# Performance work log

Measured on AMD Instinct MI355X. Metric: run time of the kernel, lower is better.

## Reference

```python
import jax, jax.numpy as jnp
import numpy as np
from jax import lax

# config (matches init_kwargs)
NUM_CLASSES = 10
SCORE_THRESH = 0.05
TOPK = 1000
DET_PER_IMG = 100
NMS_SCORE = 0.3
NMS_SIGMA = 0.5
IMG_H, IMG_W = 800.0, 1333.0
IOU_SUPPRESS = 0.8
BBOX_XFORM_CLIP = float(np.log(1000.0 / 16.0))
EPS = 1e-7


def setup_inputs() -> dict:
    key = jax.random.key(0)
    k1, k2, k3 = jax.random.split(key, 3)
    B, A, C = 8, 200000, NUM_CLASSES
    cls_logits = jax.random.normal(k1, (B, A, C), dtype=jnp.float32)
    bbox_regression = 0.5 * jax.random.normal(k2, (B, A, 4), dtype=jnp.float32)
    # plausible anchors: random centers + sizes inside the image, xyxy format
    u = jax.random.uniform(k3, (A, 6), dtype=jnp.float32)
    cx = u[:, 0] * IMG_W
    cy = u[:, 1] * IMG_H
    w = 16.0 + u[:, 2] * 200.0
    h = 16.0 + u[:, 3] * 200.0
    anchors = jnp.stack([cx - 0.5 * w, cy - 0.5 * h, cx + 0.5 * w, cy + 0.5 * h], axis=-1)
    return {"cls_logits": cls_logits, "bbox_regression": bbox_regression, "anchors": anchors}


def _decode(rel, anc):
    # torchvision BoxCoder.decode_single, weights (1,1,1,1). rel, anc: [K,4] xyxy anchors
    wa = anc[:, 2] - anc[:, 0]
    ha = anc[:, 3] - anc[:, 1]
    cxa = anc[:, 0] + 0.5 * wa
    cya = anc[:, 1] + 0.5 * ha
    dx, dy = rel[:, 0], rel[:, 1]
    dw = jnp.minimum(rel[:, 2], BBOX_XFORM_CLIP)
    dh = jnp.minimum(rel[:, 3], BBOX_XFORM_CLIP)
    cx = dx * wa + cxa
    cy = dy * ha + cya
    w = jnp.exp(dw) * wa
    h = jnp.exp(dh) * ha
    boxes = jnp.stack([cx - 0.5 * w, cy - 0.5 * h, cx + 0.5 * w, cy + 0.5 * h], axis=-1)
    # clip_boxes_to_image
    x = jnp.clip(boxes[:, 0::2], 0.0, IMG_W)
    y = jnp.clip(boxes[:, 1::2], 0.0, IMG_H)
    return jnp.stack([x[:, 0], y[:, 0], x[:, 1], y[:, 1]], axis=-1)


def _iou_one(box, boxes):
    # box [4] vs boxes [K,4] -> [K]
    lt = jnp.maximum(box[:2], boxes[:, :2])
    rb = jnp.minimum(box[2:], boxes[:, 2:])
    wh = jnp.clip(rb - lt, 0.0)
    inter = wh[:, 0] * wh[:, 1]
    a1 = (box[2] - box[0]) * (box[3] - box[1])
    a2 = (boxes[:, 2] - boxes[:, 0]) * (boxes[:, 3] - boxes[:, 1])
    return inter / (a1 + a2 - inter + EPS)


def _postprocess_one(logits, rel, anchors):
    # logits [A,C], rel [A,4], anchors [A,4]
    probs = jax.nn.sigmoid(logits)
    scores_all = jnp.max(probs, axis=-1)               # [A]
    labels_all = jnp.argmax(probs, axis=-1)            # [A]
    scores_all = jnp.where(scores_all > SCORE_THRESH, scores_all, 0.0)
    top_scores, top_idx = lax.top_k(scores_all, TOPK)  # [K]
    labels = labels_all[top_idx]
    boxes = _decode(rel[top_idx], anchors[top_idx])    # [K,4]

    K = TOPK
    # --- batched gaussian soft-NMS (same-label decay only) ---
    def soft_step(carry, _):
        sc, out = carry
        i = jnp.argmax(sc)
        s = sc[i]
        out = out.at[i].set(jnp.maximum(s, 0.0))
        ious = _iou_one(boxes[i], boxes)
        decay = jnp.where(labels == labels[i], jnp.exp(-(ious ** 2) / NMS_SIGMA), 1.0)
        sc = (sc * decay).at[i].set(-1.0)
        return (sc, out), None
    (_, decayed), _ = lax.scan(soft_step, (top_scores, jnp.zeros_like(top_scores)), None, length=K)
    keep = decayed > NMS_SCORE

    # --- sort by decayed score desc, greedy hard suppression at IoU>0.8 ---
    order = jnp.argsort(-decayed)
    b = boxes[order]
    s = decayed[order]
    l = labels[order]
    alive0 = keep[order]
    idxs = jnp.arange(K)

    def greedy_step(alive, i):
        ious = _iou_one(b[i], b)
        suppress = (ious > IOU_SUPPRESS) & (idxs > i)
        alive = jnp.where(alive[i], alive & ~suppress, alive)
        return alive, None
    alive, _ = lax.scan(greedy_step, alive0, idxs)

    final_scores = jnp.where(alive, s, -1.0)
    out_scores, out_i = lax.top_k(final_scores, DET_PER_IMG)  # preserves desc order of survivors
    return b[out_i], out_scores, l[out_i]


def reference(cls_logits, bbox_regression, anchors):
    boxes, scores, labels = jax.vmap(_postprocess_one, in_axes=(0, 0, None))(
        cls_logits, bbox_regression, anchors)
    return boxes, scores, labels  # [B,D,4], [B,D], [B,D] (score -1 = padding)
```

## Files before the change

### kernel.cpp

```cpp
#include <hip/hip_runtime.h>
#include <math.h>

#define NCLS 10
#define TOPK 1000
#define DETS 100
#define CANDMAX 4096
#define SLOTS 16
#define ACTK 256

#define NB2 256
#define MGATE (-2.9444389791664403f)
#define SEAM 2.2f
#define SCA 30.907200f
#define SCB 41.0f
#define NBLK 64

__device__ __forceinline__ float sigmoidf_(float x) {
    return 1.0f / (1.0f + expf(-x));
}

__device__ __forceinline__ int mbin_(float m) {
    if (!(m > MGATE)) return 0;
    int b;
    if (m > SEAM) { b = 161 + (int)((m - SEAM) * SCB); if (b > 255) b = 255; }
    else          { b = 1 + (int)((m - MGATE) * SCA);  if (b > 160) b = 160; }
    return b;
}

__device__ __forceinline__ float key_score(const unsigned long long* key, int c) {
    return __uint_as_float(~(unsigned)(key[c] >> 32));
}

__device__ __forceinline__ unsigned fkey_(float f) {
    unsigned b = __float_as_uint(f);
    return (b & 0x80000000u) ? ~b : (b | 0x80000000u);
}
__device__ __forceinline__ float funkey_(unsigned k) {
    return __uint_as_float((k & 0x80000000u) ? (k & 0x7FFFFFFFu) : ~k);
}

__device__ __forceinline__ unsigned wave_umax_(unsigned x) {
    unsigned t;
    t = (unsigned)__builtin_amdgcn_update_dpp(0, (int)x, 0x111, 0xF, 0xF, false); x = (x > t) ? x : t;
    t = (unsigned)__builtin_amdgcn_update_dpp(0, (int)x, 0x112, 0xF, 0xF, false); x = (x > t) ? x : t;
    t = (unsigned)__builtin_amdgcn_update_dpp(0, (int)x, 0x114, 0xF, 0xF, false); x = (x > t) ? x : t;
    t = (unsigned)__builtin_amdgcn_update_dpp(0, (int)x, 0x118, 0xF, 0xF, false); x = (x > t) ? x : t;
    t = (unsigned)__builtin_amdgcn_update_dpp(0, (int)x, 0x142, 0xF, 0xF, false); x = (x > t) ? x : t;
    t = (unsigned)__builtin_amdgcn_update_dpp(0, (int)x, 0x143, 0xF, 0xF, false); x = (x > t) ? x : t;
    return (unsigned)__builtin_amdgcn_readlane((int)x, 63);
}

__global__ __launch_bounds__(256) void k_score_bins(const float* __restrict__ logits,
                                                    unsigned char* __restrict__ binc,
                                                    unsigned* hist,
                                                    unsigned* __restrict__ done,
                                                    unsigned* __restrict__ P,
                                                    int A) {
    __shared__ unsigned h[4][NB2];
    __shared__ int s_last;
    int img = blockIdx.y;
    for (int i = threadIdx.x; i < 4 * NB2; i += 256) ((unsigned*)h)[i] = 0;
    __syncthreads();

    const float* base = logits + (size_t)img * A * NCLS;
    unsigned char* bc = binc + (size_t)img * A;
    int rep = threadIdx.x & 3;
    int nquad = A >> 2;
    for (int q = blockIdx.x * 256 + threadIdx.x; q < nquad; q += NBLK * 256) {
        const float4* lp = (const float4*)(base + (size_t)q * 40);
        float f[40];
#pragma unroll
        for (int i = 0; i < 10; ++i) ((float4*)f)[i] = lp[i];
        unsigned ub = 0;
#pragma unroll
        for (int j = 0; j < 4; ++j) {
            float m = f[10 * j];
#pragma unroll
            for (int c = 1; c < 10; ++c) m = fmaxf(m, f[10 * j + c]);
            int b = mbin_(m);
            ub |= ((unsigned)b) << (8 * j);
            if (b) atomicAdd(&h[rep][b], 1u);
        }
        *(unsigned*)(bc + (size_t)q * 4) = ub;
    }
    int tail0 = nquad << 2;
    if (blockIdx.x == 0) {
        for (int a = tail0 + (int)threadIdx.x; a < A; a += 256) {
            const float* lp2 = base + (size_t)a * NCLS;
            float m = lp2[0];
            for (int c = 1; c < 10; ++c) m = fmaxf(m, lp2[c]);
            int b = mbin_(m);
            bc[a] = (unsigned char)b;
            if (b) atomicAdd(&h[rep][b], 1u);
        }
    }
    __syncthreads();
    for (int i = threadIdx.x; i < NB2; i += 256) {
        unsigned c = h[0][i] + h[1][i] + h[2][i] + h[3][i];
        if (c) atomicAdd(&hist[(size_t)img * NB2 + i], c);
    }
    __syncthreads();
    if (threadIdx.x == 0) {
        __threadfence();
        unsigned old = atomicAdd(&done[img], 1u);
        s_last = (old == (unsigned)(NBLK - 1)) ? 1 : 0;
    }
    __syncthreads();
    if (s_last && threadIdx.x < 64) {
        int lane = threadIdx.x;
        unsigned* hh = hist + (size_t)img * NB2;
        unsigned b4[4];
        unsigned s = 0;
#pragma unroll
        for (int j = 0; j < 4; ++j) { b4[j] = atomicAdd(&hh[lane * 4 + j], 0u); s += b4[j]; }
        unsigned suf = s;
#pragma unroll
        for (int d = 1; d < 64; d <<= 1) {
            unsigned o = __shfl_down(suf, d);
            if (lane + d < 64) suf += o;
        }
        unsigned above = __shfl_down(suf, 1);
        if (lane == 63) above = 0;
        if (lane == 0 && suf < (unsigned)TOPK) P[img] = 0u;
        if (above < (unsigned)TOPK && suf >= (unsigned)TOPK) {
            unsigned cum = above;
            for (int j = 3; j >= 0; --j) {
                cum += b4[j];
                if (cum >= (unsigned)TOPK) { P[img] = (unsigned)(lane * 4 + j); break; }
            }
        }
    }
}

__global__ __launch_bounds__(256) void k_compact(const float* __restrict__ logits,
                                                 const unsigned char* __restrict__ binc,
                                                 const unsigned* __restrict__ P,
                                                 unsigned* __restrict__ ctr,
                                                 unsigned long long* __restrict__ cand,
                                                 int A) {
    int img = blockIdx.y;
    unsigned p = P[img];
    unsigned psel = p ? (p - 1u) : 0u;
    int lane = threadIdx.x & 63;
    const float* base = logits + (size_t)img * A * NCLS;
    const unsigned* b4 = (const unsigned*)(binc + (size_t)img * A);
    int nquad = A >> 2;
    for (int q = blockIdx.x * 256 + threadIdx.x; q < nquad; q += NBLK * 256) {
        unsigned ub = b4[q];
#pragma unroll
        for (int j = 0; j < 4; ++j) {
            unsigned bj = (ub >> (8 * j)) & 0xFFu;
            bool take = (psel == 0u) || (bj >= psel);
            unsigned long long mask = __ballot(take);
            if (mask) {
                int cnt = __popcll(mask);
                int leader = __ffsll((unsigned long long)mask) - 1;
                unsigned pos = 0;
                if (lane == leader) pos = atomicAdd(&ctr[img], (unsigned)cnt);
                pos = (unsigned)__shfl((int)pos, leader);
                if (take) {
                    unsigned slot = pos + (unsigned)__popcll(mask & ((1ull << lane) - 1ull));
                    if (slot < CANDMAX) {
                        unsigned a = (unsigned)(q * 4 + j);
                        const float* lp = base + (size_t)a * NCLS;
                        float m = lp[0];
#pragma unroll
                        for (int c = 1; c < 10; ++c) m = fmaxf(m, lp[c]);
                        float sc = sigmoidf_(m);
                        sc = (sc > 0.05f) ? sc : 0.0f;
                        unsigned bits = __float_as_uint(sc);
                        cand[(size_t)img * CANDMAX + slot] =
                            ((unsigned long long)bits << 32) | (unsigned)(~a);
                    }
                }
            }
        }
    }
    int tail0 = nquad << 2;
    if (blockIdx.x == 0) {
        for (int a = tail0 + (int)threadIdx.x; a < A; a += 256) {
            unsigned bj = binc[(size_t)img * A + a];
            if ((psel == 0u) || (bj >= psel)) {
                const float* lp = base + (size_t)a * NCLS;
                float m = lp[0];
                for (int c = 1; c < 10; ++c) m = fmaxf(m, lp[c]);
                float sc = sigmoidf_(m);
                sc = (sc > 0.05f) ? sc : 0.0f;
                unsigned bits = __float_as_uint(sc);
                unsigned pos = atomicAdd(&ctr[img], 1u);
                if (pos < CANDMAX)
                    cand[(size_t)img * CANDMAX + pos] =
                        ((unsigned long long)bits << 32) | (unsigned)(~a);
            }
        }
    }
}

__global__ __launch_bounds__(1024) void k_sortnms(const unsigned long long* __restrict__ cand,
                                                  const unsigned* __restrict__ ctr,
                                                  const float* __restrict__ logits,
                                                  const float* __restrict__ rel,
                                                  const float* __restrict__ anch,
                                                  float* __restrict__ out, int A, int B) {
    __shared__ unsigned long long key[CANDMAX];
    __shared__ float s_box[TOPK][4];
    __shared__ int   s_lab[TOPK];
    __shared__ float s_pbox[TOPK][4];
    __shared__ int   s_plab[TOPK];
    __shared__ float s_psc[TOPK];
    __shared__ int   s_alive[TOPK];

    const float CLIPV = 4.135166556742356f;
    const float EPS = 1e-7f;
    const float W_ = 1333.0f, H_ = 800.0f;

    int img = blockIdx.x;
    int tid = threadIdx.x;

    unsigned n = ctr[img];
    if (n > CANDMAX) n = CANDMAX;
    int L = (n <= 1024) ? 1024 : (n <= 2048) ? 2048 : CANDMAX;
    for (int i = tid; i < L; i += 1024)
        key[i] = (i < (int)n) ? ~cand[(size_t)img * CANDMAX + i] : ~0ull;
    __syncthreads();
    for (int k = 2; k <= L; k <<= 1) {
        for (int j = k >> 1; j > 0; j >>= 1) {
            for (int i = tid; i < L; i += 1024) {
                int l = i ^ j;
                if (l > i) {
                    unsigned long long va = key[i], vb = key[l];
                    bool up = ((i & k) == 0);
                    if (up ? (va > vb) : (va < vb)) { key[i] = vb; key[l] = va; }
                }
            }
            __syncthreads();
        }
    }
    for (int i = L + tid; i < CANDMAX; i += 1024) key[i] = ~0ull;
    __syncthreads();

    if (tid < TOPK) {
        unsigned long long ik = key[tid];
        unsigned ai = (unsigned)ik;
        if (ai >= (unsigned)A) ai = 0;
        const float* lp = logits + ((size_t)img * A + ai) * NCLS;
        float best = sigmoidf_(lp[0]); int lbb = 0;
#pragma unroll
        for (int cc = 1; cc < NCLS; ++cc) {
            float v = sigmoidf_(lp[cc]);
            if (v > best) { best = v; lbb = cc; }
        }
        const float* rp = rel + ((size_t)img * A + ai) * 4;
        const float* ap = anch + (size_t)ai * 4;
        float a0 = ap[0], a1 = ap[1], a2 = ap[2], a3 = ap[3];
        float wa = a2 - a0, ha = a3 - a1;
        float cxa = a0 + 0.5f * wa, cya = a1 + 0.5f * ha;
        float dx = rp[0], dy = rp[1];
        float dw = fminf(rp[2], CLIPV), dh = fminf(rp[3], CLIPV);
        float cx = dx * wa + cxa, cy = dy * ha + cya;
        float w = expf(dw) * wa, h = expf(dh) * ha;
        s_box[tid][0] = fminf(fmaxf(cx - 0.5f * w, 0.0f), W_);
        s_box[tid][1] = fminf(fmaxf(cy - 0.5f * h, 0.0f), H_);
        s_box[tid][2] = fminf(fmaxf(cx + 0.5f * w, 0.0f), W_);
        s_box[tid][3] = fminf(fmaxf(cy + 0.5f * h, 0.0f), H_);
        s_lab[tid] = lbb;
    }
    __syncthreads();
    if (tid >= 64) return;
    int lane = tid;

    int M = TOPK;
    int need_full = 0;
    float bound = key_score(key, ACTK);

    {
        float sc[4], x1[4], y1[4], x2[4], y2[4], ar[4];
        int lb[4];
#pragma unroll
        for (int j = 0; j < 4; ++j) {
            int c = lane + (j << 6);
            float4 bb = *(const float4*)&s_box[c][0];
            x1[j] = bb.x; y1[j] = bb.y; x2[j] = bb.z; y2[j] = bb.w;
            ar[j] = (bb.z - bb.x) * (bb.w - bb.y);
            lb[j] = s_lab[c];
            sc[j] = key_score(key, c);
        }

        int nconf = 0, Mf = -1;

        for (int t = 0; t < ACTK; ++t) {
            float bv = sc[0]; int bj = 0;
#pragma unroll
            for (int j = 1; j < 4; ++j)
                if (sc[j] > bv) { bv = sc[j]; bj = j; }
            unsigned mk = fkey_(bv);
            unsigned mx = wave_umax_(mk);
            float pcur = funkey_(mx);

            if (!(pcur >= bound)) { need_full = 1; break; }

            int pick = -1;
#pragma unroll
            for (int jj = 0; jj < 4; ++jj) {
                if (pick < 0) {
                    unsigned long long mj = __ballot(mk == mx && bj == jj);
                    if (mj) pick = (jj << 6) + (__ffsll(mj) - 1);
                }
            }

            int jw = pick >> 6, wl = pick & 63;
            float xs = x1[0], ys = y1[0], zs = x2[0], ws = y2[0]; int ls = lb[0];
            if (jw == 1) { xs = x1[1]; ys = y1[1]; zs = x2[1]; ws = y2[1]; ls = lb[1]; }
            if (jw == 2) { xs = x1[2]; ys = y1[2]; zs = x2[2]; ws = y2[2]; ls = lb[2]; }
            if (jw == 3) { xs = x1[3]; ys = y1[3]; zs = x2[3]; ws = y2[3]; ls = lb[3]; }
            float4 pb;
            pb.x = __int_as_float(__builtin_amdgcn_readlane(__float_as_int(xs), wl));
            pb.y = __int_as_float(__builtin_amdgcn_readlane(__float_as_int(ys), wl));
            pb.z = __int_as_float(__builtin_amdgcn_readlane(__float_as_int(zs), wl));
            pb.w = __int_as_float(__builtin_amdgcn_readlane(__float_as_int(ws), wl));
            int plab_ = __builtin_amdgcn_readlane(ls, wl);

            float psc = fmaxf(pcur, 0.0f);
            if (lane == 0) {
                *(float4*)&s_pbox[t][0] = pb;
                s_plab[t] = plab_;
                s_psc[t] = psc;
            }

            float4 qb[4]; int ga[4];
#pragma unroll
            for (int k = 0; k < 4; ++k) {
                int p = lane + (k << 6);
                int pc2 = (p < t) ? p : 0;
                qb[k] = *(const float4*)&s_pbox[pc2][0];
                ga[k] = (p < t) ? s_alive[pc2] : 0;
            }

            float wax = (pb.z - pb.x) * (pb.w - pb.y);
#pragma unroll
            for (int j = 0; j < 4; ++j) {
                float lx2 = fmaxf(pb.x, x1[j]), ly2 = fmaxf(pb.y, y1[j]);
                float rx2 = fminf(pb.z, x2[j]), ry2 = fminf(pb.w, y2[j]);
                float iw2 = fmaxf(rx2 - lx2, 0.0f), ih2 = fmaxf(ry2 - ly2, 0.0f);
                float inter2 = iw2 * ih2;
                bool hot = (inter2 > 0.0f) && (lb[j] == plab_);
                if (__ballot(hot) != 0ull) {
                    float iou2 = inter2 / (wax + ar[j] - inter2 + EPS);
                    float ie = (lb[j] == plab_) ? iou2 : 0.0f;
                    sc[j] *= expf(-(ie * ie) / 0.5f);
                }
            }
#pragma unroll
            for (int j = 0; j < 4; ++j)
                if (lane + (j << 6) == pick) sc[j] = -1.0f;

            bool sup = false;
#pragma unroll
            for (int k = 0; k < 4; ++k) {
                if (ga[k]) {
                    float lx = fmaxf(pb.x, qb[k].x), ly = fmaxf(pb.y, qb[k].y);
                    float rx = fminf(pb.z, qb[k].z), ry = fminf(pb.w, qb[k].w);
                    float iw = fmaxf(rx - lx, 0.0f), ih = fmaxf(ry - ly, 0.0f);
                    float inter = iw * ih;
                    float qa = (qb[k].z - qb[k].x) * (qb[k].w - qb[k].y);
                    float iou = inter / (wax + qa - inter + EPS);
                    sup = sup || (iou > 0.8f);
                }
            }
            bool alive = (psc > 0.3f) && (__ballot(sup) == 0ull);
            if (lane == 0) s_alive[t] = alive ? 1 : 0;
            nconf += alive ? 1 : 0;
            if (nconf >= DETS) { Mf = t + 1; break; }
        }
        if (!need_full) {
            if (Mf < 0) need_full = 1;
            else M = Mf;
        }
    }

    if (need_full) {
        float sc[SLOTS], x1[SLOTS], y1[SLOTS], x2[SLOTS], y2[SLOTS], ar[SLOTS];
        int lb[SLOTS];
#pragma unroll
        for (int j = 0; j < SLOTS; ++j) {
            int c = lane + (j << 6);
            if (c < TOPK) {
                float4 bb = *(const float4*)&s_box[c][0];
                x1[j] = bb.x; y1[j] = bb.y; x2[j] = bb.z; y2[j] = bb.w;
                ar[j] = (bb.z - bb.x) * (bb.w - bb.y);
                lb[j] = s_lab[c];
                sc[j] = key_score(key, c);
            } else {
                sc[j] = -2.0f; lb[j] = -1;
                x1[j] = y1[j] = x2[j] = y2[j] = ar[j] = 0.0f;
            }
        }
        unsigned long long aw = 0;
        if (lane < 15) aw = ~0ull;
        else if (lane == 15) aw = (1ull << (TOPK - 15 * 64)) - 1;
        int f = 0, nconf = 0;
        M = TOPK;
        for (int t = 0; t < TOPK; ++t) {
            int fp = (f < TOPK) ? f : 0;
            float4 fb = *(const float4*)&s_box[fp][0];
            int flab = s_lab[fp];
            int fs = f >> 6;
            float v = sc[0];
#pragma unroll
            for (int j = 1; j < SLOTS; ++j) if (fs == j) v = sc[j];
            float cf = __shfl(v, f & 63);
            float lm = sc[0];
#pragma unroll
            for (int j = 1; j < SLOTS; ++j) lm = fmaxf(lm, sc[j]);
            int pick; float pcur; float4 pb; int plab_;
            unsigned long long bb2 = __ballot(lm > cf);
            if (bb2 == 0) {
                pick = f; pcur = cf; pb = fb; plab_ = flab;
            } else {
                float bv = sc[0]; int bi = lane;
#pragma unroll
                for (int j = 1; j < SLOTS; ++j) {
                    int e = lane + (j << 6);
                    if (sc[j] > bv) { bv = sc[j]; bi = e; }
                }
#pragma unroll
                for (int d = 32; d; d >>= 1) {
                    float ov = __shfl_xor(bv, d);
                    int oi = __shfl_xor(bi, d);
                    if (ov > bv || (ov == bv && oi < bi)) { bv = ov; bi = oi; }
                }
                pick = bi; pcur = bv;
                pb = *(const float4*)&s_box[pick][0];
                plab_ = s_lab[pick];
            }
            float psc = fmaxf(pcur, 0.0f);
            if (lane == 0) {
                *(float4*)&s_pbox[t][0] = pb;
                s_plab[t] = plab_;
                s_psc[t] = psc;
            }
            bool alive = (psc > 0.3f);
            if (alive && t > 0) {
                float pa = (pb.z - pb.x) * (pb.w - pb.y);
                int kprev = ((t - 1) >> 6) + 1;
                bool sup = false;
                for (int k = 0; k < kprev; ++k) {
                    int p = lane + (k << 6);
                    int pc = (p < t) ? p : 0;
                    float4 qb = *(const float4*)&s_pbox[pc][0];
                    int ga = s_alive[pc];
                    if (p < t && ga) {
                        float lx = fmaxf(pb.x, qb.x), ly = fmaxf(pb.y, qb.y);
                        float rx = fminf(pb.z, qb.z), ry = fminf(pb.w, qb.w);
                        float iw = fmaxf(rx - lx, 0.0f), ih = fmaxf(ry - ly, 0.0f);
                        float inter = iw * ih;
                        float qa = (qb.z - qb.x) * (qb.w - qb.y);
                        float iou = inter / (pa + qa - inter + EPS);
                        sup = sup || (iou > 0.8f);
                    }
                }
                alive = (__ballot(sup) == 0ull);
            }
            if (lane == 0) s_alive[t] = alive ? 1 : 0;
            nconf += alive ? 1 : 0;
            if (nconf >= DETS) { M = t + 1; break; }
            float wax = (pb.z - pb.x) * (pb.w - pb.y);
#pragma unroll
            for (int j = 0; j < SLOTS; ++j) {
                float lx2 = fmaxf(pb.x, x1[j]), ly2 = fmaxf(pb.y, y1[j]);
                float rx2 = fminf(pb.z, x2[j]), ry2 = fminf(pb.w, y2[j]);
                float iw2 = fmaxf(rx2 - lx2, 0.0f), ih2 = fmaxf(ry2 - ly2, 0.0f);
                float inter2 = iw2 * ih2;
                bool hot = (inter2 > 0.0f) && (lb[j] == plab_);
                if (__ballot(hot) != 0ull) {
                    float iou2 = inter2 / (wax + ar[j] - inter2 + EPS);
                    float ie = (lb[j] == plab_) ? iou2 : 0.0f;
                    sc[j] *= expf(-(ie * ie) / 0.5f);
                }
            }
#pragma unroll
            for (int j = 0; j < SLOTS; ++j)
                if (lane + (j << 6) == pick) sc[j] = -1.0f;
            if (lane == (pick >> 6)) aw &= ~(1ull << (pick & 63));
            if (pick == f) {
                int fw = f >> 6;
                unsigned long long w2 = __shfl(aw, fw);
                while (w2 == 0ull && fw < 15) { ++fw; w2 = __shfl(aw, fw); }
                f = (w2 == 0ull) ? TOPK : (fw << 6) + (__ffsll(w2) - 1);
            }
        }
    }

    float* out_boxes  = out;
    float* out_scores = out + (size_t)B * DETS * 4;
    float* out_labels = out + (size_t)B * DETS * 5;
    int kmax = (M + 63) >> 6;
    int base = 0;
    for (int k = 0; k < kmax; ++k) {
        int p = lane + (k << 6);
        bool av = (p < M) && (s_alive[p] != 0);
        unsigned long long mask = __ballot(av);
        int slot = base + (int)__popcll(mask & ((1ull << lane) - 1ull));
        if (av && slot < DETS) {
            float4 pb = *(const float4*)&s_pbox[p][0];
            float* ob = out_boxes + ((size_t)img * DETS + slot) * 4;
            ob[0] = pb.x; ob[1] = pb.y; ob[2] = pb.z; ob[3] = pb.w;
            out_scores[img * DETS + slot] = s_psc[p];
            out_labels[img * DETS + slot] = (float)s_plab[p];
        }
        base += (int)__popcll(mask);
    }
    if (base < DETS) {
        int dbase = 0;
        for (int k = 0; k < kmax; ++k) {
            int p = lane + (k << 6);
            bool dd = (p < M) && (s_alive[p] == 0);
            unsigned long long mask = __ballot(dd);
            int slot = base + dbase + (int)__popcll(mask & ((1ull << lane) - 1ull));
            if (dd && slot < DETS) {
                float4 pb = *(const float4*)&s_pbox[p][0];
                float* ob = out_boxes + ((size_t)img * DETS + slot) * 4;
                ob[0] = pb.x; ob[1] = pb.y; ob[2] = pb.z; ob[3] = pb.w;
                out_scores[img * DETS + slot] = -1.0f;
                out_labels[img * DETS + slot] = (float)s_plab[p];
            }
            dbase += (int)__popcll(mask);
        }
    }
}

extern "C" void kernel_launch(void* const* d_in, const int* in_sizes, int n_in,
                              void* d_out, int out_size, void* d_ws, size_t ws_size,
                              hipStream_t stream) {
    const float* logits = (const float*)d_in[0];
    const float* rel = (const float*)d_in[1];
    const float* anch = (const float*)d_in[2];
    float* out = (float*)d_out;

    int A = in_sizes[2] / 4;
    int B = in_sizes[0] / (A * NCLS);

    char* w = (char*)d_ws;
    unsigned* hist = (unsigned*)w;           w += (size_t)B * NB2 * 4;
    unsigned* ctr = (unsigned*)w;            w += (size_t)B * 4;
    unsigned* done = (unsigned*)w;           w += (size_t)B * 4;
    size_t zbytes = (size_t)(w - (char*)d_ws);
    unsigned long long* cand = (unsigned long long*)w; w += (size_t)B * CANDMAX * 8;
    unsigned* P = (unsigned*)w;              w += (size_t)B * 4;
    unsigned char* binc = (unsigned char*)w;

    hipMemsetAsync(d_ws, 0, zbytes, stream);

    dim3 g1(NBLK, (unsigned)B);
    k_score_bins<<<g1, 256, 0, stream>>>(logits, binc, hist, done, P, A);
    k_compact<<<g1, 256, 0, stream>>>(logits, binc, P, ctr, cand, A);
    k_sortnms<<<B, 1024, 0, stream>>>(cand, ctr, logits, rel, anch, out, A, B);
}
```

Measured before the change: 273.0 us.

## Stage logits tiles through LDS for coalesced loads; read picked box from shared

The score-binning kernel now loads a 256-anchor tile of logits cooperatively with coalesced float4 loads into shared memory, then each thread reduces one anchor's 10 classes from LDS. Previously each thread issued ten strided float4 loads for four anchors. The aim is better global-memory coalescing, at the cost of two block barriers per tile and byte-wide bin stores. Separately, the soft-NMS pick now reads the selected box and label from shared arrays instead of using a select chain plus readlanes, which assumes s_box/s_lab hold the candidates.

```diff
diff --git a/kernel.cpp b/kernel.cpp
--- a/kernel.cpp
+++ b/kernel.cpp
@@ -7,6 +7,7 @@
 #define CANDMAX 4096
 #define SLOTS 16
 #define ACTK 256
+#define TILE 256
 
 #define NB2 256
 #define MGATE (-2.9444389791664403f)
@@ -56,36 +57,39 @@
                                                     unsigned* __restrict__ done,
                                                     unsigned* __restrict__ P,
                                                     int A) {
+    __shared__ float tilef[TILE * NCLS];
     __shared__ unsigned h[4][NB2];
     __shared__ int s_last;
     int img = blockIdx.y;
-    for (int i = threadIdx.x; i < 4 * NB2; i += 256) ((unsigned*)h)[i] = 0;
+    int tid = threadIdx.x;
+    for (int i = tid; i < 4 * NB2; i += 256) ((unsigned*)h)[i] = 0;
     __syncthreads();
 
     const float* base = logits + (size_t)img * A * NCLS;
     unsigned char* bc = binc + (size_t)img * A;
-    int rep = threadIdx.x & 3;
-    int nquad = A >> 2;
-    for (int q = blockIdx.x * 256 + threadIdx.x; q < nquad; q += NBLK * 256) {
-        const float4* lp = (const float4*)(base + (size_t)q * 40);
-        float f[40];
-#pragma unroll
-        for (int i = 0; i < 10; ++i) ((float4*)f)[i] = lp[i];
-        unsigned ub = 0;
-#pragma unroll
-        for (int j = 0; j < 4; ++j) {
-            float m = f[10 * j];
-#pragma unroll
-            for (int c = 1; c < 10; ++c) m = fmaxf(m, f[10 * j + c]);
-            int b = mbin_(m);
-            ub |= ((unsigned)b) << (8 * j);
-            if (b) atomicAdd(&h[rep][b], 1u);
-        }
-        *(unsigned*)(bc + (size_t)q * 4) = ub;
-    }
-    int tail0 = nquad << 2;
+    int rep = tid & 3;
+
+    int ntile = A / TILE;
+    for (int tile = blockIdx.x; tile < ntile; tile += NBLK) {
+        const float4* src = (const float4*)(base + (size_t)tile * TILE * NCLS);
+        float4 v0 = src[tid];
+        float4 v1 = src[256 + tid];
+        float4 v2;
+        if (tid < 128) v2 = src[512 + tid];
+        ((float4*)tilef)[tid] = v0;
+        ((float4*)tilef)[256 + tid] = v1;
+        if (tid < 128) ((float4*)tilef)[512 + tid] = v2;
+        __syncthreads();
+        float m = tilef[tid * 10];
+#pragma unroll
+        for (int c = 1; c < 10; ++c) m = fmaxf(m, tilef[tid * 10 + c]);
+        int b = mbin_(m);
+        bc[(size_t)tile * TILE + tid] = (unsigned char)b;
+        if (b) atomicAdd(&h[rep][b], 1u);
+        __syncthreads();
+    }
     if (blockIdx.x == 0) {
-        for (int a = tail0 + (int)threadIdx.x; a < A; a += 256) {
+        for (int a = ntile * TILE + tid; a < A; a += 256) {
             const float* lp2 = base + (size_t)a * NCLS;
             float m = lp2[0];
             for (int c = 1; c < 10; ++c) m = fmaxf(m, lp2[c]);
@@ -95,19 +99,19 @@
         }
     }
     __syncthreads();
-    for (int i = threadIdx.x; i < NB2; i += 256) {
+    for (int i = tid; i < NB2; i += 256) {
         unsigned c = h[0][i] + h[1][i] + h[2][i] + h[3][i];
         if (c) atomicAdd(&hist[(size_t)img * NB2 + i], c);
     }
     __syncthreads();
-    if (threadIdx.x == 0) {
+    if (tid == 0) {
         __threadfence();
         unsigned old = atomicAdd(&done[img], 1u);
         s_last = (old == (unsigned)(NBLK - 1)) ? 1 : 0;
     }
     __syncthreads();
-    if (s_last && threadIdx.x < 64) {
-        int lane = threadIdx.x;
+    if (s_last && tid < 64) {
+        int lane = tid;
         unsigned* hh = hist + (size_t)img * NB2;
         unsigned b4[4];
         unsigned s = 0;
@@ -308,19 +312,9 @@
                 }
             }
 
-            int jw = pick >> 6, wl = pick & 63;
-            float xs = x1[0], ys = y1[0], zs = x2[0], ws = y2[0]; int ls = lb[0];
-            if (jw == 1) { xs = x1[1]; ys = y1[1]; zs = x2[1]; ws = y2[1]; ls = lb[1]; }
-            if (jw == 2) { xs = x1[2]; ys = y1[2]; zs = x2[2]; ws = y2[2]; ls = lb[2]; }
-            if (jw == 3) { xs = x1[3]; ys = y1[3]; zs = x2[3]; ws = y2[3]; ls = lb[3]; }
-            float4 pb;
-            pb.x = __int_as_float(__builtin_amdgcn_readlane(__float_as_int(xs), wl));
-            pb.y = __int_as_float(__builtin_amdgcn_readlane(__float_as_int(ys), wl));
-            pb.z = __int_as_float(__builtin_amdgcn_readlane(__float_as_int(zs), wl));
-            pb.w = __int_as_float(__builtin_amdgcn_readlane(__float_as_int(ws), wl));
-            int plab_ = __builtin_amdgcn_readlane(ls, wl);
-
             float psc = fmaxf(pcur, 0.0f);
+            float4 pb = *(const float4*)&s_box[pick][0];
+            int plab_ = s_lab[pick];
             if (lane == 0) {
                 *(float4*)&s_pbox[t][0] = pb;
                 s_plab[t] = plab_;
```

After: 258.1 us. -5.4%, faster.
